# Performance work log

Hardware: AMD Instinct MI355X
Metric: run time of the kernel (lower is better)

Reference implementation:

```python
import jax, jax.numpy as jnp
import numpy as np

B, S, D, H, HID = 8, 1024, 768, 12, 3072
HD = D // H
EPS = 1e-5


def layernorm(x, g, b):
    mu = jnp.mean(x, axis=-1, keepdims=True)
    var = jnp.mean(jnp.square(x - mu), axis=-1, keepdims=True)
    return (x - mu) * jax.lax.rsqrt(var + EPS) * g + b


def setup_inputs() -> dict:
    key = jax.random.key(0)
    ks = jax.random.split(key, 8)
    s_d = 1.0 / np.sqrt(D)
    s_h = 1.0 / np.sqrt(HID)
    return {
        "x": jax.random.normal(ks[0], (B, S, D), jnp.float32),
        # attention projections (stored as [in, out])
        "wq": jax.random.normal(ks[1], (D, D), jnp.float32) * s_d,
        "bq": jnp.zeros((D,), jnp.float32),
        "wk": jax.random.normal(ks[2], (D, D), jnp.float32) * s_d,
        "bk": jnp.zeros((D,), jnp.float32),
        "wv": jax.random.normal(ks[3], (D, D), jnp.float32) * s_d,
        "bv": jnp.zeros((D,), jnp.float32),
        # layernorms
        "ln1_g": jnp.ones((D,), jnp.float32),
        "ln1_b": jnp.zeros((D,), jnp.float32),
        "ln2_g": jnp.ones((D,), jnp.float32),
        "ln2_b": jnp.zeros((D,), jnp.float32),
        # MLP
        "w_in": jax.random.normal(ks[4], (D, HID), jnp.float32) * s_d,
        "b_in": jnp.zeros((HID,), jnp.float32),
        "w_out": jax.random.normal(ks[5], (HID, D), jnp.float32) * s_h,
        "b_out": jnp.zeros((D,), jnp.float32),
    }


def reference(x, wq, bq, wk, bk, wv, bv, ln1_g, ln1_b, ln2_g, ln2_b,
              w_in, b_in, w_out, b_out):
    scale = HD ** -0.5
    # --- MHSA (note: original forward never applies out_proj) ---
    q = (x @ wq + bq).reshape(B, S, H, HD).transpose(0, 2, 1, 3)  # [B,H,S,hd]
    k = (x @ wk + bk).reshape(B, S, H, HD).transpose(0, 2, 1, 3)
    v = (x @ wv + bv).reshape(B, S, H, HD).transpose(0, 2, 1, 3)
    scores = jnp.einsum("bhqd,bhkd->bhqk", q, k)  # full NxN, as in source
    attn = jax.nn.softmax(scores * scale, axis=-1)
    ctx = jnp.einsum("bhqk,bhkd->bhqd", attn, v)
    ctx = ctx.transpose(0, 2, 1, 3).reshape(B, S, D)
    # --- residual: pre_ln applied to attention OUTPUT (as in source) ---
    x = x + layernorm(ctx, ln1_g, ln1_b)
    # --- MLP: GELU after BOTH linears (as in source), dropout=0 ---
    h = jax.nn.gelu(layernorm(x, ln2_g, ln2_b) @ w_in + b_in, approximate=False)
    h = jax.nn.gelu(h @ w_out + b_out, approximate=False)
    return x + h
```

## Files before the change

### kernel.cpp

```cpp
#include <hip/hip_runtime.h>
#include <math.h>

typedef __attribute__((ext_vector_type(8))) short short8;
typedef __attribute__((ext_vector_type(4))) short short4v;
typedef __attribute__((ext_vector_type(4))) float f32x4;

#define MFMA16(a, b, c) __builtin_amdgcn_mfma_f32_16x16x32_bf16(a, b, c, 0, 0, 0)

__device__ __forceinline__ short f2bf(float f) {
    union { float f; unsigned u; } v; v.f = f;
    unsigned r = v.u + 0x7fffu + ((v.u >> 16) & 1u);
    return (short)(r >> 16);
}
__device__ __forceinline__ float bf2f(short s) {
    union { unsigned u; float f; } v; v.u = ((unsigned)(unsigned short)s) << 16;
    return v.f;
}
__device__ __forceinline__ float gelu(float v) {
    float u = v * (1.0f + 0.044715f * v * v);
    float e = exp2f(-2.3021184f * u);
    return v * __builtin_amdgcn_rcpf(1.0f + e);
}
__device__ __forceinline__ void async16(const short* g, short* l) {
    __builtin_amdgcn_global_load_lds((const __attribute__((address_space(1))) void*)g,
                                     (__attribute__((address_space(3))) void*)l, 16, 0, 0);
}

__device__ __forceinline__ short8 build_pfrag(int lg, float x0, float x1, float x2, float x3,
                                              float x4, float x5, float x6, float x7) {
    unsigned a0, a1, b0, b1;
    asm("v_cvt_pk_bf16_f32 %0, %1, %2" : "=v"(a0) : "v"(x0), "v"(x1));
    asm("v_cvt_pk_bf16_f32 %0, %1, %2" : "=v"(a1) : "v"(x2), "v"(x3));
    asm("v_cvt_pk_bf16_f32 %0, %1, %2" : "=v"(b0) : "v"(x4), "v"(x5));
    asm("v_cvt_pk_bf16_f32 %0, %1, %2" : "=v"(b1) : "v"(x6), "v"(x7));
    unsigned u0 = (lg < 2) ? b0 : a0, u1 = (lg < 2) ? b1 : a1;
    unsigned v0 = (unsigned)__shfl_xor((int)u0, 32), v1 = (unsigned)__shfl_xor((int)u1, 32);
    unsigned w0 = (lg < 2) ? a0 : b0, w1 = (lg < 2) ? a1 : b1;
    bool sw = ((lg ^ (lg >> 1)) & 1) != 0;
    unsigned s0 = sw ? w0 : v0, s1 = sw ? w1 : v1;
    unsigned r0 = (unsigned)__shfl_xor((int)s0, 16), r1 = (unsigned)__shfl_xor((int)s1, 16);
    union { unsigned u[4]; short8 s; } o;
    o.u[0] = (lg & 1) ? r0 : ((lg == 0) ? w0 : v0);
    o.u[1] = (lg & 1) ? r1 : ((lg == 0) ? w1 : v1);
    o.u[2] = (lg & 1) ? ((lg == 1) ? v0 : w0) : r0;
    o.u[3] = (lg & 1) ? ((lg == 1) ? v1 : w1) : r1;
    return o.s;
}

__global__ __launch_bounds__(256) void cast_kernel(const float* __restrict__ in,
                                                   short* __restrict__ out, int n4) {
    int i = blockIdx.x * 256 + threadIdx.x;
    if (i < n4) {
        float4 v = ((const float4*)in)[i];
        short4v o;
        o.x = f2bf(v.x); o.y = f2bf(v.y); o.z = f2bf(v.z); o.w = f2bf(v.w);
        ((short4v*)out)[i] = o;
    }
}

__global__ __launch_bounds__(256) void concat_bias(const float* __restrict__ a,
                                                   const float* __restrict__ b,
                                                   const float* __restrict__ c,
                                                   float* __restrict__ o) {
    int i = blockIdx.x * 256 + threadIdx.x;
    if (i < 768) o[i] = a[i];
    else if (i < 1536) o[i] = b[i - 768];
    else if (i < 2304) o[i] = c[i - 1536];
}

__global__ __launch_bounds__(256) void transpose_cast(const float* __restrict__ in,
                                                      short* __restrict__ out,
                                                      int K, int N) {
    __shared__ float tile[32][33];
    int n0 = blockIdx.x * 32, k0 = blockIdx.y * 32;
    int tx = threadIdx.x & 31, ty = threadIdx.x >> 5;
#pragma unroll
    for (int r = 0; r < 4; ++r)
        tile[ty + r * 8][tx] = in[(size_t)(k0 + ty + r * 8) * N + n0 + tx];
    __syncthreads();
#pragma unroll
    for (int r = 0; r < 4; ++r) {
        int rr = ty + r * 8;
        out[(size_t)(n0 + rr) * K + k0 + tx] = f2bf(tile[tx][rr]);
    }
}

__global__ __launch_bounds__(256) void transpose_v(const short* __restrict__ in,
                                                   short* __restrict__ out) {
    __shared__ short tile[32][33];
    const int bh = blockIdx.z;
    const int s0 = blockIdx.y * 32, d0 = blockIdx.x * 32;
    const short* src = in + (size_t)bh * 1024 * 64;
    short* dst = out + (size_t)bh * 64 * 1024;
    int tx = threadIdx.x & 31, ty = threadIdx.x >> 5;
#pragma unroll
    for (int r = 0; r < 4; ++r)
        tile[ty + r * 8][tx] = src[(size_t)(s0 + ty + r * 8) * 64 + d0 + tx];
    __syncthreads();
#pragma unroll
    for (int r = 0; r < 4; ++r) {
        int rr = ty + r * 8;
        dst[(size_t)(d0 + rr) * 1024 + s0 + tx] = tile[tx][rr];
    }
}

template <int EPI, int NF>
__global__ __launch_bounds__(256) void gemm_kernel(const short* __restrict__ A,
                                                   const short* __restrict__ Bt,
                                                   const float* __restrict__ bias,
                                                   void* __restrict__ Cout,
                                                   const float* __restrict__ resid,
                                                   int M, int N, int K) {
    const int TN = NF * 32;
    const int t = threadIdx.x;
    const int wid = t >> 6, lane = t & 63;
    const int wm = wid >> 1, wn = wid & 1;
    const int lr = lane & 15, lg = lane >> 4;
    const int row0 = blockIdx.y * 128, col0 = blockIdx.x * TN;

    __shared__ __align__(16) short As[128 * 64];
    __shared__ __align__(16) short Bs[NF * 32 * 64];

    f32x4 acc[4][NF];
#pragma unroll
    for (int i = 0; i < 4; ++i)
#pragma unroll
        for (int j = 0; j < NF; ++j) acc[i][j] = (f32x4){0.f, 0.f, 0.f, 0.f};

    const int aRow = wid * 8 + (lane >> 3);
    const int aK = ((lane & 7) ^ (lane >> 3)) << 3;
    const short* Ag = A + (size_t)(row0 + aRow) * K + aK;
    const short* Bg = Bt + (size_t)(col0 + aRow) * K + aK;
    short* AsW = As + wid * 8 * 64;
    short* BsW = Bs + wid * 8 * 64;
    const int swz = lr & 7;

    for (int k0 = 0; k0 < K; k0 += 64) {
        __syncthreads();
#pragma unroll
        for (int j = 0; j < 4; ++j)
            async16(Ag + (size_t)(j * 32) * K + k0, AsW + j * 32 * 64);
#pragma unroll
        for (int j = 0; j < NF; ++j)
            async16(Bg + (size_t)(j * 32) * K + k0, BsW + j * 32 * 64);
        __syncthreads();

#pragma unroll
        for (int ks = 0; ks < 2; ++ks) {
            const int rdofs = ((ks * 4 + lg) ^ swz) << 3;
            short8 af[4], bfr[NF];
#pragma unroll
            for (int i = 0; i < 4; ++i)
                af[i] = *(short8*)(As + (wm * 64 + i * 16 + lr) * 64 + rdofs);
#pragma unroll
            for (int i = 0; i < NF; ++i)
                bfr[i] = *(short8*)(Bs + (wn * (NF * 16) + i * 16 + lr) * 64 + rdofs);
#pragma unroll
            for (int mi = 0; mi < 4; ++mi)
#pragma unroll
                for (int ni = 0; ni < NF; ++ni)
                    acc[mi][ni] = MFMA16(af[mi], bfr[ni], acc[mi][ni]);
        }
    }

#pragma unroll
    for (int mi = 0; mi < 4; ++mi)
#pragma unroll
        for (int ni = 0; ni < NF; ++ni)
#pragma unroll
            for (int r = 0; r < 4; ++r) {
                int row = row0 + wm * 64 + mi * 16 + lg * 4 + r;
                int col = col0 + wn * (NF * 16) + ni * 16 + lr;
                float v = acc[mi][ni][r] + bias[col];
                if constexpr (EPI == 0) {
                    unsigned uc = (unsigned)col;
                    unsigned m = uc / 768u;
                    unsigned rest = uc - m * 768u;
                    unsigned h = rest >> 6, d = rest & 63u;
                    int b = row >> 10, s_ = row & 1023;
                    ((short*)Cout)[((((size_t)m * 96 + (size_t)b * 12 + h) * 1024 + s_) * 64) + d] = f2bf(v);
                } else if constexpr (EPI == 1) {
                    ((short*)Cout)[(size_t)row * N + col] = f2bf(gelu(v));
                } else {
                    size_t idx = (size_t)row * N + col;
                    ((float*)Cout)[idx] = resid[idx] + gelu(v);
                }
            }
}

__global__ __launch_bounds__(256) void attn_kernel(const short* __restrict__ Q,
                                                   const short* __restrict__ Kg,
                                                   const short* __restrict__ VTg,
                                                   short* __restrict__ ctx) {
    const int bh = blockIdx.x;
    const int q0 = blockIdx.y * 64;
    const int t = threadIdx.x, wid = t >> 6, lane = t & 63;
    const int lr = lane & 15, lg = lane >> 4;
    const float C = 0.18033688011f;

    __shared__ __align__(16) short Qs[64][72];
    __shared__ __align__(16) short Ks[64][72];
    __shared__ __align__(16) short Vt[64][72];

    const size_t base = (size_t)bh * 1024 * 64;
    const size_t vbase = (size_t)bh * 64 * 1024;

#pragma unroll
    for (int pass = 0; pass < 2; ++pass) {
        int slot = pass * 256 + t;
        int r = slot >> 3, ds = (slot & 7) << 3;
        *(short8*)&Qs[r][ds] = *(const short8*)(Q + base + (size_t)(q0 + r) * 64 + ds);
    }
    __syncthreads();
    short8 qf[2];
    qf[0] = *(short8*)&Qs[wid * 16 + lr][lg * 8];
    qf[1] = *(short8*)&Qs[wid * 16 + lr][32 + lg * 8];

    f32x4 oacc[4];
#pragma unroll
    for (int i = 0; i < 4; ++i) oacc[i] = (f32x4){0.f, 0.f, 0.f, 0.f};
    float mrun = -1e30f, lrun = 0.f;

    for (int kt = 0; kt < 16; ++kt) {
        __syncthreads();
        const int krow0 = kt * 64;
#pragma unroll
        for (int pass = 0; pass < 2; ++pass) {
            int slot = pass * 256 + t;
            int r = slot >> 3, ds = (slot & 7) << 3;
            *(short8*)&Ks[r][ds] = *(const short8*)(Kg + base + (size_t)(krow0 + r) * 64 + ds);
            *(short8*)&Vt[r][ds] = *(const short8*)(VTg + vbase + (size_t)r * 1024 + krow0 + ds);
        }
        __syncthreads();

        f32x4 sfr[4];
#pragma unroll
        for (int cf = 0; cf < 4; ++cf) {
            f32x4 s = (f32x4){0.f, 0.f, 0.f, 0.f};
            short8 kf0 = *(short8*)&Ks[cf * 16 + lr][lg * 8];
            short8 kf1 = *(short8*)&Ks[cf * 16 + lr][32 + lg * 8];
            s = MFMA16(kf0, qf[0], s);
            s = MFMA16(kf1, qf[1], s);
            sfr[cf] = s;
        }

        float tv[16];
#pragma unroll
        for (int cf = 0; cf < 4; ++cf)
#pragma unroll
            for (int r = 0; r < 4; ++r) tv[cf * 4 + r] = sfr[cf][r] * C;
        float mx = tv[0];
#pragma unroll
        for (int i = 1; i < 16; ++i) mx = fmaxf(mx, tv[i]);
        mx = fmaxf(mx, __shfl_xor(mx, 16));
        mx = fmaxf(mx, __shfl_xor(mx, 32));
        float mnew = fmaxf(mrun, mx);
        float fac = exp2f(mrun - mnew);
        float p[16];
        float rs = 0.f;
#pragma unroll
        for (int i = 0; i < 16; ++i) { p[i] = exp2f(tv[i] - mnew); rs += p[i]; }
        rs += __shfl_xor(rs, 16);
        rs += __shfl_xor(rs, 32);
        lrun = lrun * fac + rs;
        mrun = mnew;

#pragma unroll
        for (int r = 0; r < 4; ++r) {
            float fr = __shfl(fac, lg * 4 + r);
#pragma unroll
            for (int df = 0; df < 4; ++df) oacc[df][r] *= fr;
        }

        short8 pf0 = build_pfrag(lg, p[0], p[1], p[2], p[3], p[4], p[5], p[6], p[7]);
        short8 pf1 = build_pfrag(lg, p[8], p[9], p[10], p[11], p[12], p[13], p[14], p[15]);
#pragma unroll
        for (int df = 0; df < 4; ++df) {
            short8 vf0 = *(short8*)&Vt[df * 16 + lr][lg * 8];
            oacc[df] = MFMA16(pf0, vf0, oacc[df]);
        }
#pragma unroll
        for (int df = 0; df < 4; ++df) {
            short8 vf1 = *(short8*)&Vt[df * 16 + lr][32 + lg * 8];
            oacc[df] = MFMA16(pf1, vf1, oacc[df]);
        }
    }

    const int b = bh / 12, h = bh % 12;
    float rinv[4];
#pragma unroll
    for (int r = 0; r < 4; ++r) {
        float lr_ = __shfl(lrun, lg * 4 + r);
        rinv[r] = __builtin_amdgcn_rcpf(lr_);
    }
#pragma unroll
    for (int df = 0; df < 4; ++df)
#pragma unroll
        for (int r = 0; r < 4; ++r) {
            int q = q0 + wid * 16 + lg * 4 + r;
            int d = df * 16 + lr;
            float o = oacc[df][r] * rinv[r];
            ctx[((size_t)b * 1024 + q) * 768 + h * 64 + d] = f2bf(o);
        }
}

__global__ __launch_bounds__(256) void ln_fused(const float* __restrict__ x,
                                                const short* __restrict__ ctx,
                                                const float* __restrict__ g1,
                                                const float* __restrict__ b1,
                                                const float* __restrict__ g2,
                                                const float* __restrict__ b2,
                                                float* __restrict__ x2,
                                                short* __restrict__ ln2b) {
    const int row = blockIdx.x, t = threadIdx.x;
    const int wid = t >> 6, lane = t & 63;
    __shared__ float red[8];

    float c[3], xv[3];
#pragma unroll
    for (int j = 0; j < 3; ++j) {
        int idx = t + 256 * j;
        c[j] = bf2f(ctx[(size_t)row * 768 + idx]);
        xv[j] = x[(size_t)row * 768 + idx];
    }
    float s = c[0] + c[1] + c[2];
    float s2 = c[0] * c[0] + c[1] * c[1] + c[2] * c[2];
#pragma unroll
    for (int off = 32; off > 0; off >>= 1) { s += __shfl_down(s, off); s2 += __shfl_down(s2, off); }
    if (lane == 0) { red[wid] = s; red[4 + wid] = s2; }
    __syncthreads();
    s = red[0] + red[1] + red[2] + red[3];
    s2 = red[4] + red[5] + red[6] + red[7];
    float mu = s * (1.0f / 768.0f);
    float rstd = rsqrtf(s2 * (1.0f / 768.0f) - mu * mu + 1e-5f);

    float y[3];
#pragma unroll
    for (int j = 0; j < 3; ++j) {
        int idx = t + 256 * j;
        y[j] = xv[j] + (c[j] - mu) * rstd * g1[idx] + b1[idx];
        x2[(size_t)row * 768 + idx] = y[j];
    }
    __syncthreads();
    s = y[0] + y[1] + y[2];
    s2 = y[0] * y[0] + y[1] * y[1] + y[2] * y[2];
#pragma unroll
    for (int off = 32; off > 0; off >>= 1) { s += __shfl_down(s, off); s2 += __shfl_down(s2, off); }
    if (lane == 0) { red[wid] = s; red[4 + wid] = s2; }
    __syncthreads();
    s = red[0] + red[1] + red[2] + red[3];
    s2 = red[4] + red[5] + red[6] + red[7];
    float mu2 = s * (1.0f / 768.0f);
    float rstd2 = rsqrtf(s2 * (1.0f / 768.0f) - mu2 * mu2 + 1e-5f);
#pragma unroll
    for (int j = 0; j < 3; ++j) {
        int idx = t + 256 * j;
        ln2b[(size_t)row * 768 + idx] = f2bf((y[j] - mu2) * rstd2 * g2[idx] + b2[idx]);
    }
}

extern "C" void kernel_launch(void* const* d_in, const int* in_sizes, int n_in,
                              void* d_out, int out_size, void* d_ws, size_t ws_size,
                              hipStream_t stream) {
    const float* x    = (const float*)d_in[0];
    const float* wq   = (const float*)d_in[1];
    const float* bq   = (const float*)d_in[2];
    const float* wk   = (const float*)d_in[3];
    const float* bk   = (const float*)d_in[4];
    const float* wv   = (const float*)d_in[5];
    const float* bv   = (const float*)d_in[6];
    const float* g1   = (const float*)d_in[7];
    const float* b1   = (const float*)d_in[8];
    const float* g2   = (const float*)d_in[9];
    const float* b2   = (const float*)d_in[10];
    const float* w_in = (const float*)d_in[11];
    const float* b_in = (const float*)d_in[12];
    const float* w_out  = (const float*)d_in[13];
    const float* b_out  = (const float*)d_in[14];
    float* out = (float*)d_out;

    char* ws = (char*)d_ws;
    short* xb     = (short*)(ws + 0);
    short* vT     = (short*)(ws + 0);
    short* qb     = (short*)(ws + 12582912);
    short* kb     = (short*)(ws + 25165824);
    short* vb     = (short*)(ws + 37748736);
    short* h1     = (short*)(ws + 0);
    short* ctx    = (short*)(ws + 50331648);
    float* x2     = (float*)(ws + 62914560);
    float* bqkv   = (float*)(ws + 62914560);
    short* ln2b   = (short*)(ws + 88080384);
    short* wqkvT  = (short*)(ws + 100663296);
    short* w_inT  = (short*)(ws + 104202240);
    short* w_outT = (short*)(ws + 108920832);

    cast_kernel<<<6144, 256, 0, stream>>>(x, xb, 1572864);
    concat_bias<<<9, 256, 0, stream>>>(bq, bk, bv, bqkv);
    transpose_cast<<<dim3(24, 24), 256, 0, stream>>>(wq, wqkvT, 768, 768);
    transpose_cast<<<dim3(24, 24), 256, 0, stream>>>(wk, wqkvT + 768 * 768, 768, 768);
    transpose_cast<<<dim3(24, 24), 256, 0, stream>>>(wv, wqkvT + 2 * 768 * 768, 768, 768);
    transpose_cast<<<dim3(96, 24), 256, 0, stream>>>(w_in, w_inT, 768, 3072);
    transpose_cast<<<dim3(24, 96), 256, 0, stream>>>(w_out, w_outT, 3072, 768);

    gemm_kernel<0, 4><<<dim3(18, 64), 256, 0, stream>>>(xb, wqkvT, bqkv, qb, nullptr, 8192, 2304, 768);

    transpose_v<<<dim3(2, 32, 96), 256, 0, stream>>>(vb, vT);

    attn_kernel<<<dim3(96, 16), 256, 0, stream>>>(qb, kb, vT, ctx);

    ln_fused<<<8192, 256, 0, stream>>>(x, ctx, g1, b1, g2, b2, x2, ln2b);

    gemm_kernel<1, 4><<<dim3(24, 64), 256, 0, stream>>>(ln2b, w_inT, b_in, h1, nullptr, 8192, 3072, 768);
    gemm_kernel<2, 4><<<dim3(6, 64), 256, 0, stream>>>(h1, w_outT, b_out, out, x2, 8192, 768, 3072);
}
```

Before: 392.2 us.

## Use async LDS loads with XOR swizzle, fold softmax scale into Q, lazy rescale

```diff
diff --git a/kernel.cpp b/kernel.cpp
--- a/kernel.cpp
+++ b/kernel.cpp
@@ -20,6 +20,9 @@
     float u = v * (1.0f + 0.044715f * v * v);
     float e = exp2f(-2.3021184f * u);
     return v * __builtin_amdgcn_rcpf(1.0f + e);
+}
+__device__ __forceinline__ float max3f(float a, float b, float c) {
+    float d; asm("v_max3_f32 %0, %1, %2, %3" : "=v"(d) : "v"(a), "v"(b), "v"(c)); return d;
 }
 __device__ __forceinline__ void async16(const short* g, short* l) {
     __builtin_amdgcn_global_load_lds((const __attribute__((address_space(1))) void*)g,
@@ -178,6 +181,7 @@
                     unsigned rest = uc - m * 768u;
                     unsigned h = rest >> 6, d = rest & 63u;
                     int b = row >> 10, s_ = row & 1023;
+                    if (m == 0u) v *= 0.18033688011f;
                     ((short*)Cout)[((((size_t)m * 96 + (size_t)b * 12 + h) * 1024 + s_) * 64) + d] = f2bf(v);
                 } else if constexpr (EPI == 1) {
                     ((short*)Cout)[(size_t)row * N + col] = f2bf(gelu(v));
@@ -196,92 +200,103 @@
     const int q0 = blockIdx.y * 64;
     const int t = threadIdx.x, wid = t >> 6, lane = t & 63;
     const int lr = lane & 15, lg = lane >> 4;
-    const float C = 0.18033688011f;
-
-    __shared__ __align__(16) short Qs[64][72];
-    __shared__ __align__(16) short Ks[64][72];
-    __shared__ __align__(16) short Vt[64][72];
+
+    __shared__ __align__(16) short Qs[64 * 64];
+    __shared__ __align__(16) short Ks[64 * 64];
+    __shared__ __align__(16) short Vt[64 * 64];
 
     const size_t base = (size_t)bh * 1024 * 64;
     const size_t vbase = (size_t)bh * 64 * 1024;
 
-#pragma unroll
-    for (int pass = 0; pass < 2; ++pass) {
-        int slot = pass * 256 + t;
-        int r = slot >> 3, ds = (slot & 7) << 3;
-        *(short8*)&Qs[r][ds] = *(const short8*)(Q + base + (size_t)(q0 + r) * 64 + ds);
+    const int srow = lane >> 3;
+    const int lslot8 = ((lane & 7) ^ srow) << 3;
+    const int r0w = wid * 16;
+    const int swz = lr & 7;
+
+    {
+        const short* g = Q + base + (size_t)(q0 + r0w + srow) * 64 + lslot8;
+        async16(g, Qs + r0w * 64);
+        async16(g + 8 * 64, Qs + (r0w + 8) * 64);
     }
     __syncthreads();
     short8 qf[2];
-    qf[0] = *(short8*)&Qs[wid * 16 + lr][lg * 8];
-    qf[1] = *(short8*)&Qs[wid * 16 + lr][32 + lg * 8];
+    qf[0] = *(short8*)(Qs + (r0w + lr) * 64 + ((lg ^ swz) << 3));
+    qf[1] = *(short8*)(Qs + (r0w + lr) * 64 + (((4 + lg) ^ swz) << 3));
 
     f32x4 oacc[4];
 #pragma unroll
     for (int i = 0; i < 4; ++i) oacc[i] = (f32x4){0.f, 0.f, 0.f, 0.f};
     float mrun = -1e30f, lrun = 0.f;
 
+    const short* kg = Kg + base + (size_t)(r0w + srow) * 64 + lslot8;
+    const short* vg = VTg + vbase + (size_t)(r0w + srow) * 1024 + lslot8;
+
     for (int kt = 0; kt < 16; ++kt) {
+        const int krow0 = kt * 64;
         __syncthreads();
-        const int krow0 = kt * 64;
-#pragma unroll
-        for (int pass = 0; pass < 2; ++pass) {
-            int slot = pass * 256 + t;
-            int r = slot >> 3, ds = (slot & 7) << 3;
-            *(short8*)&Ks[r][ds] = *(const short8*)(Kg + base + (size_t)(krow0 + r) * 64 + ds);
-            *(short8*)&Vt[r][ds] = *(const short8*)(VTg + vbase + (size_t)r * 1024 + krow0 + ds);
-        }
+        async16(kg + (size_t)krow0 * 64, Ks + r0w * 64);
+        async16(kg + (size_t)(krow0 + 8) * 64, Ks + (r0w + 8) * 64);
+        async16(vg + krow0, Vt + r0w * 64);
+        async16(vg + krow0 + 8 * 1024, Vt + (r0w + 8) * 64);
         __syncthreads();
 
         f32x4 sfr[4];
 #pragma unroll
         for (int cf = 0; cf < 4; ++cf) {
             f32x4 s = (f32x4){0.f, 0.f, 0.f, 0.f};
-            short8 kf0 = *(short8*)&Ks[cf * 16 + lr][lg * 8];
-            short8 kf1 = *(short8*)&Ks[cf * 16 + lr][32 + lg * 8];
+            short8 kf0 = *(short8*)(Ks + (cf * 16 + lr) * 64 + ((lg ^ swz) << 3));
+            short8 kf1 = *(short8*)(Ks + (cf * 16 + lr) * 64 + (((4 + lg) ^ swz) << 3));
             s = MFMA16(kf0, qf[0], s);
             s = MFMA16(kf1, qf[1], s);
             sfr[cf] = s;
         }
 
-        float tv[16];
-#pragma unroll
-        for (int cf = 0; cf < 4; ++cf)
-#pragma unroll
-            for (int r = 0; r < 4; ++r) tv[cf * 4 + r] = sfr[cf][r] * C;
-        float mx = tv[0];
-#pragma unroll
-        for (int i = 1; i < 16; ++i) mx = fmaxf(mx, tv[i]);
+        float g0 = max3f(sfr[0][0], sfr[0][1], sfr[0][2]);
+        float g1 = max3f(sfr[0][3], sfr[1][0], sfr[1][1]);
+        float g2 = max3f(sfr[1][2], sfr[1][3], sfr[2][0]);
+        float g3 = max3f(sfr[2][1], sfr[2][2], sfr[2][3]);
+        float g4 = max3f(sfr[3][0], sfr[3][1], sfr[3][2]);
+        float mx = fmaxf(max3f(g0, g1, g2), max3f(g3, g4, sfr[3][3]));
         mx = fmaxf(mx, __shfl_xor(mx, 16));
         mx = fmaxf(mx, __shfl_xor(mx, 32));
-        float mnew = fmaxf(mrun, mx);
-        float fac = exp2f(mrun - mnew);
+
+        if (!__all(mx <= mrun + 8.0f)) {
+            float mnew = fmaxf(mrun, mx);
+            float fac = exp2f(mrun - mnew);
+            lrun *= fac;
+#pragma unroll
+            for (int r = 0; r < 4; ++r) {
+                float fr = __shfl(fac, lg * 4 + r);
+#pragma unroll
+                for (int df = 0; df < 4; ++df) oacc[df][r] *= fr;
+            }
+            mrun = mnew;
+        }
+
         float p[16];
-        float rs = 0.f;
-#pragma unroll
-        for (int i = 0; i < 16; ++i) { p[i] = exp2f(tv[i] - mnew); rs += p[i]; }
+#pragma unroll
+        for (int cf = 0; cf < 4; ++cf)
+#pragma unroll
+            for (int r = 0; r < 4; ++r) p[cf * 4 + r] = exp2f(sfr[cf][r] - mrun);
+        float s0 = (p[0] + p[1]) + (p[2] + p[3]);
+        float s1 = (p[4] + p[5]) + (p[6] + p[7]);
+        float s2 = (p[8] + p[9]) + (p[10] + p[11]);
+        float s3 = (p[12] + p[13]) + (p[14] + p[15]);
+        float rs = (s0 + s1) + (s2 + s3);
         rs += __shfl_xor(rs, 16);
         rs += __shfl_xor(rs, 32);
-        lrun = lrun * fac + rs;
-        mrun = mnew;
-
-#pragma unroll
-        for (int r = 0; r < 4; ++r) {
-            float fr = __shfl(fac, lg * 4 + r);
-#pragma unroll
-            for (int df = 0; df < 4; ++df) oacc[df][r] *= fr;
-        }
+        lrun += rs;
 
         short8 pf0 = build_pfrag(lg, p[0], p[1], p[2], p[3], p[4], p[5], p[6], p[7]);
         short8 pf1 = build_pfrag(lg, p[8], p[9], p[10], p[11], p[12], p[13], p[14], p[15]);
 #pragma unroll
         for (int df = 0; df < 4; ++df) {
-            short8 vf0 = *(short8*)&Vt[df * 16 + lr][lg * 8];
+            short8 vf0 = *(short8*)(Vt + (df * 16 + lr) * 64 + ((lg ^ swz) << 3));
             oacc[df] = MFMA16(pf0, vf0, oacc[df]);
         }
 #pragma unroll
         for (int df = 0; df < 4; ++df) {
-            short8 vf1 = *(short8*)&Vt[df * 16 + lr][32 + lg * 8];
+            short8 vf1 = *(short8*)(Vt + (df * 16 + lr) * 64 + (((4 + lg) ^ swz) << 3));
             oacc[df] = MFMA16(pf1, vf1, oacc[df]);
         }
     }
```

After: 397.1 us. Within noise of the previous version (+1.2%).
